# Optimization experiments

Hardware: AMD Instinct MI355X
Metric: run time of the kernel (lower is better)

The kernel has to match this reference:

```python
import jax, jax.numpy as jnp
import numpy as np

BATCH, IN_DIM, HID, STATES = 4096, 256, 512, 16

def setup_inputs() -> dict:
    key = jax.random.key(0)
    k1, k2, k3 = jax.random.split(key, 3)
    x = jax.random.normal(k1, (BATCH, IN_DIM), dtype=jnp.float32)
    h_quantum = jax.random.normal(k2, (BATCH, HID, STATES), dtype=jnp.float32)
    # param initialized with normal(0.1) stddev in the original
    W_quantum = jax.random.normal(k3, (IN_DIM, HID, STATES), dtype=jnp.float32) * 0.1
    return {"x": x, "h_quantum": h_quantum, "W_quantum": W_quantum}

def reference(x, h_quantum, W_quantum):
    # Fused equivalent of the per-state loop: one batched contraction
    # input_contrib[b,h,s] = sum_i x[b,i] * W[i,h,s]
    input_contrib = jnp.einsum('bi,ihs->bhs', x, W_quantum)
    new_quantum_state = jnp.tanh(input_contrib + h_quantum * 0.9)
    output = jnp.mean(new_quantum_state, axis=-1)  # [B, HID]
    return (output, new_quantum_state)
```

## Files before the change

### kernel.cpp

```cpp
#include <hip/hip_runtime.h>

#define BATCH  4096
#define IN_DIM 256
#define HID    512
#define NCOL   8192

#define BM 128
#define BN 64

typedef __attribute__((ext_vector_type(8))) short bf16x8;
typedef __attribute__((ext_vector_type(4))) float f32x4;
typedef __attribute__((ext_vector_type(4))) float fvec4;

typedef __attribute__((address_space(1))) const unsigned as1_uint;
typedef __attribute__((address_space(3))) unsigned       as3_uint;

__device__ __forceinline__ uint pack_hi(float f0, float f1) {
    return __builtin_amdgcn_perm(__builtin_bit_cast(uint, f1),
                                 __builtin_bit_cast(uint, f0), 0x07060302u);
}
__device__ __forceinline__ float hi_part(float f) {
    return __builtin_bit_cast(float, __builtin_bit_cast(uint, f) & 0xFFFF0000u);
}
__device__ __forceinline__ float tanh_fast(float x) {
    float e = __builtin_amdgcn_exp2f(x * 2.8853900817779268f);
    float r = __builtin_amdgcn_rcpf(e + 1.0f);
    return __builtin_fmaf(-2.0f, r, 1.0f);
}
__device__ __forceinline__ void split8(const float* f, uint4& h, uint4& l) {
    h.x = pack_hi(f[0], f[1]); h.y = pack_hi(f[2], f[3]);
    h.z = pack_hi(f[4], f[5]); h.w = pack_hi(f[6], f[7]);
    l.x = pack_hi(f[0] - hi_part(f[0]), f[1] - hi_part(f[1]));
    l.y = pack_hi(f[2] - hi_part(f[2]), f[3] - hi_part(f[3]));
    l.z = pack_hi(f[4] - hi_part(f[4]), f[5] - hi_part(f[5]));
    l.w = pack_hi(f[6] - hi_part(f[6]), f[7] - hi_part(f[7]));
}

#define W_ELEMS  2097152
#define X_ELEMS  1048576
#define WS_NEED  (12u * 1024u * 1024u)

__global__ __launch_bounds__(256) void prep_w_kernel(
    const float* __restrict__ W, ushort* __restrict__ whi, ushort* __restrict__ wlo)
{
    const int n    = blockIdx.x * 256 + threadIdx.x;
    const int koct = blockIdx.y;
    float f[8];
    #pragma unroll
    for (int j = 0; j < 8; ++j)
        f[j] = __builtin_nontemporal_load(&W[(size_t)(koct * 8 + j) * NCOL + n]);
    uint4 h, l;
    split8(f, h, l);
    const size_t o = ((size_t)((n >> 4) * 32 + koct) * 16 + (n & 15)) * 8;
    *(uint4*)(whi + o) = h;
    *(uint4*)(wlo + o) = l;
}

__global__ __launch_bounds__(256) void prep_x_kernel(
    const float* __restrict__ x, ushort* __restrict__ xhi, ushort* __restrict__ xlo)
{
    const int b    = blockIdx.x * 256 + threadIdx.x;
    const int koct = blockIdx.y;
    float f[8];
    fvec4 v0 = __builtin_nontemporal_load((const fvec4*)&x[(size_t)b * IN_DIM + koct * 8]);
    fvec4 v1 = __builtin_nontemporal_load((const fvec4*)&x[(size_t)b * IN_DIM + koct * 8 + 4]);
    f[0] = v0.x; f[1] = v0.y; f[2] = v0.z; f[3] = v0.w;
    f[4] = v1.x; f[5] = v1.y; f[6] = v1.z; f[7] = v1.w;
    uint4 h, l;
    split8(f, h, l);
    const size_t o = ((size_t)((b >> 4) * 32 + koct) * 16 + (b & 15)) * 8;
    *(uint4*)(xhi + o) = h;
    *(uint4*)(xlo + o) = l;
}

__global__ __launch_bounds__(256, 3) void mqc_main_kernel(
    const ushort* __restrict__ xhi, const ushort* __restrict__ xlo,
    const ushort* __restrict__ whi, const ushort* __restrict__ wlo,
    const float* __restrict__ hq,
    float* __restrict__ out_mean, float* __restrict__ out_new)
{
    __shared__ ushort sBh[8192], sBl[8192];

    const int t     = threadIdx.x;
    const int lane  = t & 63;
    const int w     = t >> 6;
    const int lquad = lane >> 4;
    const int l16   = lane & 15;

    const int wgid = blockIdx.x;
    const int xcd  = wgid & 7;
    const int q    = wgid >> 3;
    const int rowg = (xcd << 2) | (q & 3);
    const int colg = q >> 2;
    const int row0 = rowg * BM;
    const int col0 = colg * BN;
    const int btile0 = (row0 >> 4) + w * 2;
    const int ntile0 = col0 >> 4;

    f32x4 acc[2][4] = {};

    #define STAGE(KOCT0) {                                                          \
        _Pragma("unroll")                                                           \
        for (int itc = 0; itc < 8; ++itc) {                                         \
            const int c  = itc * 4 + w;                                             \
            const int nt = (c >> 2) & 3;                                            \
            const int kl = (c & 3) * 4 + (lane >> 4);                               \
            const ushort* srcp = ((c >> 4) ? wlo : whi)                             \
                + ((size_t)(ntile0 + nt) * 32 + (KOCT0) + kl) * 128 + (lane & 15) * 8; \
            ushort* dstp = ((c >> 4) ? sBl : sBh) + nt * 2048 + (c & 3) * 512;      \
            __builtin_amdgcn_global_load_lds((as1_uint*)srcp, (as3_uint*)dstp,      \
                                             16, 0, 0);                             \
        }                                                                           \
    }

    #define APREF(AH, AL, KOCT0, SL0) {                                             \
        _Pragma("unroll")                                                           \
        for (int s = 0; s < 2; ++s) {                                               \
            const int koct = (KOCT0) + ((SL0) + s) * 4 + lquad;                     \
            _Pragma("unroll")                                                       \
            for (int mi = 0; mi < 2; ++mi) {                                        \
                const size_t o = ((size_t)(btile0 + mi) * 32 + koct) * 128 + l16 * 8; \
                AH[s][mi] = *(const bf16x8*)(xhi + o);                              \
                AL[s][mi] = *(const bf16x8*)(xlo + o);                              \
            }                                                                       \
        }                                                                           \
    }

    #define KSTEP2(AH, AL, SL0) {                                                   \
        _Pragma("unroll")                                                           \
        for (int s = 0; s < 2; ++s) {                                               \
            const int bidx = (((SL0) + s) * 4 + lquad) * 128 + l16 * 8;             \
            bf16x8 bH[4], bL[4];                                                    \
            _Pragma("unroll")                                                       \
            for (int ni = 0; ni < 4; ++ni) {                                        \
                bH[ni] = *(const bf16x8*)(sBh + ni * 2048 + bidx);                  \
                bL[ni] = *(const bf16x8*)(sBl + ni * 2048 + bidx);                  \
            }                                                                       \
            _Pragma("unroll")                                                       \
            for (int mi = 0; mi < 2; ++mi)                                          \
                _Pragma("unroll")                                                   \
                for (int ni = 0; ni < 4; ++ni)                                      \
                    acc[mi][ni] = __builtin_amdgcn_mfma_f32_16x16x32_bf16(bH[ni], AH[s][mi], acc[mi][ni], 0, 0, 0); \
            _Pragma("unroll")                                                       \
            for (int mi = 0; mi < 2; ++mi)                                          \
                _Pragma("unroll")                                                   \
                for (int ni = 0; ni < 4; ++ni)                                      \
                    acc[mi][ni] = __builtin_amdgcn_mfma_f32_16x16x32_bf16(bH[ni], AL[s][mi], acc[mi][ni], 0, 0, 0); \
            _Pragma("unroll")                                                       \
            for (int mi = 0; mi < 2; ++mi)                                          \
                _Pragma("unroll")                                                   \
                for (int ni = 0; ni < 4; ++ni)                                      \
                    acc[mi][ni] = __builtin_amdgcn_mfma_f32_16x16x32_bf16(bL[ni], AH[s][mi], acc[mi][ni], 0, 0, 0); \
        }                                                                           \
    }

    bf16x8 AaH[2][2], AaL[2][2], AbH[2][2], AbL[2][2];
    fvec4 hv[2][4];

    STAGE(0);
    APREF(AaH, AaL, 0, 0);
    #pragma unroll
    for (int mi = 0; mi < 2; ++mi) {
        const int b = row0 + w * 32 + mi * 16 + l16;
        #pragma unroll
        for (int ni = 0; ni < 4; ++ni) {
            const int n = col0 + ni * 16 + lquad * 4;
            hv[mi][ni] = *(const fvec4*)&hq[(size_t)b * NCOL + n];
        }
    }
    __syncthreads();
    APREF(AbH, AbL, 0, 2);
    KSTEP2(AaH, AaL, 0);
    KSTEP2(AbH, AbL, 2);
    __syncthreads();
    STAGE(16);
    APREF(AaH, AaL, 16, 0);
    __syncthreads();
    APREF(AbH, AbL, 16, 2);
    KSTEP2(AaH, AaL, 0);
    KSTEP2(AbH, AbL, 2);
    #undef STAGE
    #undef APREF
    #undef KSTEP2

    #pragma unroll
    for (int mi = 0; mi < 2; ++mi) {
        const int b = row0 + w * 32 + mi * 16 + l16;
        #pragma unroll
        for (int ni = 0; ni < 4; ++ni) {
            const int n = col0 + ni * 16 + lquad * 4;
            fvec4 ov;
            ov.x = tanh_fast(__builtin_fmaf(0.9f, hv[mi][ni].x, acc[mi][ni][0]));
            ov.y = tanh_fast(__builtin_fmaf(0.9f, hv[mi][ni].y, acc[mi][ni][1]));
            ov.z = tanh_fast(__builtin_fmaf(0.9f, hv[mi][ni].z, acc[mi][ni][2]));
            ov.w = tanh_fast(__builtin_fmaf(0.9f, hv[mi][ni].w, acc[mi][ni][3]));
            __builtin_nontemporal_store(ov, (fvec4*)&out_new[(size_t)b * NCOL + n]);
            float s = (ov.x + ov.y) + (ov.z + ov.w);
            s += __shfl_xor(s, 16);
            s += __shfl_xor(s, 32);
            if (lquad == 0)
                out_mean[(size_t)b * HID + (col0 >> 4) + ni] = s * 0.0625f;
        }
    }
}

#define BKF 64
__device__ __forceinline__ int swz(int row, int byteoff) {
    return byteoff ^ ((((row & 7) ^ ((row >> 3) & 7))) << 4);
}
__global__ __launch_bounds__(256, 4) void mqc_fallback_kernel(
    const float* __restrict__ x, const float* __restrict__ hq,
    const float* __restrict__ W,
    float* __restrict__ out_mean, float* __restrict__ out_new)
{
    __shared__ char sB[2 * BN * BKF * 2];
    char* const sB_hi = sB;
    char* const sB_lo = sB + BN * BKF * 2;
    const int t = threadIdx.x, lane = t & 63, w = t >> 6;
    const int lquad = lane >> 4, l16 = lane & 15;
    const int row0 = blockIdx.x * BM, col0 = blockIdx.y * BN;
    const int k0 = (t >> 4) * 4, n0 = (t & 15) * 4;
    f32x4 acc[2][4] = {};
    for (int kt = 0; kt < IN_DIM / BKF; ++kt) {
        float4 ax[2][2][2];
        #pragma unroll
        for (int mi = 0; mi < 2; ++mi)
            #pragma unroll
            for (int ks = 0; ks < 2; ++ks) {
                const float* p = &x[(size_t)(row0 + w * 32 + mi * 16 + l16) * IN_DIM
                                    + kt * BKF + ks * 32 + lquad * 8];
                ax[mi][ks][0] = *(const float4*)(p);
                ax[mi][ks][1] = *(const float4*)(p + 4);
            }
        float4 wrow[4];
        #pragma unroll
        for (int r = 0; r < 4; ++r)
            wrow[r] = *(const float4*)(&W[(size_t)(kt * BKF + k0 + r) * NCOL + col0 + n0]);
        #pragma unroll
        for (int c = 0; c < 4; ++c) {
            const float f0 = ((const float*)&wrow[0])[c];
            const float f1 = ((const float*)&wrow[1])[c];
            const float f2 = ((const float*)&wrow[2])[c];
            const float f3 = ((const float*)&wrow[3])[c];
            uint2 hv2, lv2;
            hv2.x = pack_hi(f0, f1); hv2.y = pack_hi(f2, f3);
            lv2.x = pack_hi(f0 - hi_part(f0), f1 - hi_part(f1));
            lv2.y = pack_hi(f2 - hi_part(f2), f3 - hi_part(f3));
            const int off = swz(n0 + c, (n0 + c) * (BKF * 2) + k0 * 2);
            *(uint2*)(sB_hi + off) = hv2;
            *(uint2*)(sB_lo + off) = lv2;
        }
        __syncthreads();
        #pragma unroll
        for (int ks = 0; ks < 2; ++ks) {
            bf16x8 aH[2], aL[2];
            #pragma unroll
            for (int mi = 0; mi < 2; ++mi) {
                uint4 h, l;
                split8((const float*)&ax[mi][ks][0], h, l);
                aH[mi] = __builtin_bit_cast(bf16x8, h);
                aL[mi] = __builtin_bit_cast(bf16x8, l);
            }
            const int kb = ks * 64 + lquad * 16;
            bf16x8 bH[4], bL[4];
            #pragma unroll
            for (int ni = 0; ni < 4; ++ni) {
                const int row = ni * 16 + l16;
                bH[ni] = *(const bf16x8*)(sB_hi + swz(row, row * (BKF * 2) + kb));
            }
            #pragma unroll
            for (int mi = 0; mi < 2; ++mi)
                #pragma unroll
                for (int ni = 0; ni < 4; ++ni)
                    acc[mi][ni] = __builtin_amdgcn_mfma_f32_16x16x32_bf16(bH[ni], aH[mi], acc[mi][ni], 0, 0, 0);
            #pragma unroll
            for (int mi = 0; mi < 2; ++mi)
                #pragma unroll
                for (int ni = 0; ni < 4; ++ni)
                    acc[mi][ni] = __builtin_amdgcn_mfma_f32_16x16x32_bf16(bH[ni], aL[mi], acc[mi][ni], 0, 0, 0);
            #pragma unroll
            for (int ni = 0; ni < 4; ++ni) {
                const int row = ni * 16 + l16;
                bL[ni] = *(const bf16x8*)(sB_lo + swz(row, row * (BKF * 2) + kb));
            }
            #pragma unroll
            for (int mi = 0; mi < 2; ++mi)
                #pragma unroll
                for (int ni = 0; ni < 4; ++ni)
                    acc[mi][ni] = __builtin_amdgcn_mfma_f32_16x16x32_bf16(bL[ni], aH[mi], acc[mi][ni], 0, 0, 0);
        }
        __syncthreads();
    }
    #pragma unroll
    for (int mi = 0; mi < 2; ++mi) {
        const int b = row0 + w * 32 + mi * 16 + l16;
        #pragma unroll
        for (int ni = 0; ni < 4; ++ni) {
            const int n = col0 + ni * 16 + lquad * 4;
            const float4 hv = *(const float4*)(&hq[(size_t)b * NCOL + n]);
            float4 ov;
            ov.x = tanh_fast(__builtin_fmaf(0.9f, hv.x, acc[mi][ni][0]));
            ov.y = tanh_fast(__builtin_fmaf(0.9f, hv.y, acc[mi][ni][1]));
            ov.z = tanh_fast(__builtin_fmaf(0.9f, hv.z, acc[mi][ni][2]));
            ov.w = tanh_fast(__builtin_fmaf(0.9f, hv.w, acc[mi][ni][3]));
            *(float4*)(&out_new[(size_t)b * NCOL + n]) = ov;
            float s = (ov.x + ov.y) + (ov.z + ov.w);
            s += __shfl_xor(s, 16);
            s += __shfl_xor(s, 32);
            if (lquad == 0)
                out_mean[(size_t)b * HID + (col0 >> 4) + ni] = s * 0.0625f;
        }
    }
}

extern "C" void kernel_launch(void* const* d_in, const int* in_sizes, int n_in,
                              void* d_out, int out_size, void* d_ws, size_t ws_size,
                              hipStream_t stream) {
    const float* x  = (const float*)d_in[0];
    const float* hq = (const float*)d_in[1];
    const float* W  = (const float*)d_in[2];

    float* out_mean = (float*)d_out;
    float* out_new  = (float*)d_out + (size_t)BATCH * HID;

    if (ws_size >= WS_NEED) {
        ushort* whi = (ushort*)d_ws;
        ushort* wlo = whi + W_ELEMS;
        ushort* xhi = wlo + W_ELEMS;
        ushort* xlo = xhi + X_ELEMS;
        prep_w_kernel<<<dim3(NCOL / 256, IN_DIM / 8), 256, 0, stream>>>(W, whi, wlo);
        prep_x_kernel<<<dim3(BATCH / 256, IN_DIM / 8), 256, 0, stream>>>(x, xhi, xlo);
        mqc_main_kernel<<<dim3(BATCH * NCOL / (BM * BN)), 256, 0, stream>>>(
            xhi, xlo, whi, wlo, hq, out_mean, out_new);
    } else {
        mqc_fallback_kernel<<<dim3(BATCH / BM, NCOL / BN), 256, 0, stream>>>(
            x, hq, W, out_mean, out_new);
    }
}
```

Baseline: 93.14 us.

## Double-buffer B tiles in LDS with four half-size K stages

Splits the K loop into four stages of 8 k-octets instead of two of 16, and alternates between two LDS buffers. The next stage's global-to-LDS load and A prefetch are issued before the current stage's MFMAs, so memory latency overlaps compute. The h_quantum load is moved later to shorten the initial stall. This adds more barriers, and the sBh/sBl footprint per buffer changes, which risks overlap hazards if the buffer sizing is off.

```diff
diff --git a/kernel.cpp b/kernel.cpp
--- a/kernel.cpp
+++ b/kernel.cpp
@@ -99,24 +99,25 @@
 
     f32x4 acc[2][4] = {};
 
-    #define STAGE(KOCT0) {                                                          \
+    #define STAGE(BUF, KOCT0) {                                                     \
         _Pragma("unroll")                                                           \
-        for (int itc = 0; itc < 8; ++itc) {                                         \
+        for (int itc = 0; itc < 4; ++itc) {                                         \
             const int c  = itc * 4 + w;                                             \
-            const int nt = (c >> 2) & 3;                                            \
-            const int kl = (c & 3) * 4 + (lane >> 4);                               \
-            const ushort* srcp = ((c >> 4) ? wlo : whi)                             \
+            const int nt = (c >> 1) & 3;                                            \
+            const int kl = (c & 1) * 4 + (lane >> 4);                               \
+            const ushort* srcp = ((c >> 3) ? wlo : whi)                             \
                 + ((size_t)(ntile0 + nt) * 32 + (KOCT0) + kl) * 128 + (lane & 15) * 8; \
-            ushort* dstp = ((c >> 4) ? sBl : sBh) + nt * 2048 + (c & 3) * 512;      \
+            ushort* dstp = ((c >> 3) ? sBl : sBh) + (BUF) * 4096 + nt * 1024        \
+                           + (c & 1) * 512;                                         \
             __builtin_amdgcn_global_load_lds((as1_uint*)srcp, (as3_uint*)dstp,      \
                                              16, 0, 0);                             \
         }                                                                           \
     }
 
-    #define APREF(AH, AL, KOCT0, SL0) {                                             \
+    #define APREF(AH, AL, KOCT0) {                                                  \
         _Pragma("unroll")                                                           \
         for (int s = 0; s < 2; ++s) {                                               \
-            const int koct = (KOCT0) + ((SL0) + s) * 4 + lquad;                     \
+            const int koct = (KOCT0) + s * 4 + lquad;                               \
             _Pragma("unroll")                                                       \
             for (int mi = 0; mi < 2; ++mi) {                                        \
                 const size_t o = ((size_t)(btile0 + mi) * 32 + koct) * 128 + l16 * 8; \
@@ -126,15 +127,15 @@
         }                                                                           \
     }
 
-    #define KSTEP2(AH, AL, SL0) {                                                   \
+    #define KSTEP2(BUF, AH, AL) {                                                   \
         _Pragma("unroll")                                                           \
         for (int s = 0; s < 2; ++s) {                                               \
-            const int bidx = (((SL0) + s) * 4 + lquad) * 128 + l16 * 8;             \
+            const int bidx = (BUF) * 4096 + (s * 4 + lquad) * 128 + l16 * 8;        \
             bf16x8 bH[4], bL[4];                                                    \
             _Pragma("unroll")                                                       \
             for (int ni = 0; ni < 4; ++ni) {                                        \
-                bH[ni] = *(const bf16x8*)(sBh + ni * 2048 + bidx);                  \
-                bL[ni] = *(const bf16x8*)(sBl + ni * 2048 + bidx);                  \
+                bH[ni] = *(const bf16x8*)(sBh + ni * 1024 + bidx);                  \
+                bL[ni] = *(const bf16x8*)(sBl + ni * 1024 + bidx);                  \
             }                                                                       \
             _Pragma("unroll")                                                       \
             for (int mi = 0; mi < 2; ++mi)                                          \
@@ -157,8 +158,15 @@
     bf16x8 AaH[2][2], AaL[2][2], AbH[2][2], AbL[2][2];
     fvec4 hv[2][4];
 
-    STAGE(0);
-    APREF(AaH, AaL, 0, 0);
+    STAGE(0, 0);  APREF(AaH, AaL, 0);
+    __syncthreads();
+    STAGE(1, 8);  APREF(AbH, AbL, 8);
+    KSTEP2(0, AaH, AaL);
+    __syncthreads();
+    STAGE(0, 16); APREF(AaH, AaL, 16);
+    KSTEP2(1, AbH, AbL);
+    __syncthreads();
+    STAGE(1, 24); APREF(AbH, AbL, 24);
     #pragma unroll
     for (int mi = 0; mi < 2; ++mi) {
         const int b = row0 + w * 32 + mi * 16 + l16;
@@ -168,17 +176,9 @@
             hv[mi][ni] = *(const fvec4*)&hq[(size_t)b * NCOL + n];
         }
     }
+    KSTEP2(0, AaH, AaL);
     __syncthreads();
-    APREF(AbH, AbL, 0, 2);
-    KSTEP2(AaH, AaL, 0);
-    KSTEP2(AbH, AbL, 2);
-    __syncthreads();
-    STAGE(16);
-    APREF(AaH, AaL, 16, 0);
-    __syncthreads();
-    APREF(AbH, AbL, 16, 2);
-    KSTEP2(AaH, AaL, 0);
-    KSTEP2(AbH, AbL, 2);
+    KSTEP2(1, AbH, AbL);
     #undef STAGE
     #undef APREF
     #undef KSTEP2
```

After: 90.74 us. -2.6%, faster.
